# Kernel tuning notes

Measured on AMD Instinct MI355X. Metric: run time of the kernel, lower is better.

## Reference

```python
import jax, jax.numpy as jnp
import numpy as np

DIM = 512
A_HEADS = 8
C_HEADS = 4
DH = 64
EPS = 1e-5


def layer_norm(x, g, b):
    mu = jnp.mean(x, axis=-1, keepdims=True)
    var = jnp.var(x, axis=-1, keepdims=True)
    return (x - mu) * jax.lax.rsqrt(var + EPS) * g + b


def setup_inputs() -> dict:
    key = jax.random.key(0)
    ks = jax.random.split(key, 8)
    inner_a = A_HEADS * DH  # 512
    inner_c = C_HEADS * DH  # 256
    s = 0.02
    return {
        "x": jax.random.normal(ks[0], (4, 192, DIM), dtype=jnp.float32),
        # Attention branch params
        "ln1_g": jnp.ones((DIM,), jnp.float32),
        "ln1_b": jnp.zeros((DIM,), jnp.float32),
        "Wqkv": jax.random.normal(ks[1], (DIM, 3 * inner_a), jnp.float32) * s,
        "Wo": jax.random.normal(ks[2], (inner_a, DIM), jnp.float32) * s,
        "bo": jnp.zeros((DIM,), jnp.float32),
        # Trittention branch params
        "ln2_g": jnp.ones((DIM,), jnp.float32),
        "ln2_b": jnp.zeros((DIM,), jnp.float32),
        "Wabcde": jax.random.normal(ks[3], (DIM, 5 * inner_c), jnp.float32) * s,
        "babcde": jnp.zeros((5 * inner_c,), jnp.float32),
        "Wp": jax.random.normal(ks[4], (inner_c, DIM), jnp.float32) * s,
        "bp": jnp.zeros((DIM,), jnp.float32),
    }


def _attention(x, ln_g, ln_b, Wqkv, Wo, bo):
    B, T, _ = x.shape
    xn = layer_norm(x, ln_g, ln_b)
    qkv = xn @ Wqkv  # [B,T,3*H*D]
    q, k, v = jnp.split(qkv, 3, axis=-1)
    def heads(t):
        return t.reshape(B, T, A_HEADS, DH).transpose(0, 2, 1, 3)  # [B,H,T,D]
    q, k, v = heads(q), heads(k), heads(v)
    scale = DH ** -0.5
    dots = jnp.einsum('bhqd,bhkd->bhqk', q, k) * scale
    attn = jax.nn.softmax(dots, axis=-1)
    out = jnp.einsum('bhqk,bhkd->bhqd', attn, v)
    out = out.transpose(0, 2, 1, 3).reshape(B, T, A_HEADS * DH)
    return out @ Wo + bo


def _trittention(x, ln_g, ln_b, Wabcde, babcde, Wp, bp):
    B, T, _ = x.shape
    xn = layer_norm(x, ln_g, ln_b)
    proj = xn @ Wabcde + babcde  # [B,T,5*H*D]
    a, b_, c, d_, e = jnp.split(proj, 5, axis=-1)
    def heads(t):
        return t.reshape(B, T, C_HEADS, DH)  # [B,T,H,D]
    a, b_, c, d_, e = heads(a), heads(b_), heads(c), heads(d_), heads(e)
    # cubic score: [B,H,S,T,Q]
    score = jnp.einsum('bshd,bthd,bqhd->bhstq', a, b_, c) / DH
    # softmax over joint (s,t) for each query q
    score = score.transpose(0, 1, 4, 2, 3).reshape(B, C_HEADS, T, T * T)
    attn = jax.nn.softmax(score, axis=-1).reshape(B, C_HEADS, T, T, T)
    z = (jnp.einsum('bhqst,bshd->bhqd', attn, d_)
         + jnp.einsum('bhqst,bthd->bhqd', attn, e))
    z = z.transpose(0, 2, 1, 3).reshape(B, T, C_HEADS * DH)
    return z @ Wp + bp


def reference(x, ln1_g, ln1_b, Wqkv, Wo, bo, ln2_g, ln2_b, Wabcde, babcde, Wp, bp):
    return (_attention(x, ln1_g, ln1_b, Wqkv, Wo, bo)
            + _trittention(x, ln2_g, ln2_b, Wabcde, babcde, Wp, bp))
```

## Files before the change

### kernel.cpp

```cpp
#include <hip/hip_runtime.h>
#include <cstdint>


#define B_   4
#define T_   192
#define DIM_ 512
#define AH   8
#define CH   4

typedef unsigned short u16;
typedef unsigned int   u32;
typedef __attribute__((ext_vector_type(8))) short short8;
typedef __attribute__((ext_vector_type(4))) float floatx4;
typedef __attribute__((ext_vector_type(4))) int intx4;
typedef __attribute__((ext_vector_type(2))) float f32x2;
typedef __attribute__((ext_vector_type(8))) _Float16 half8;
typedef __attribute__((ext_vector_type(2))) _Float16 half2v;
typedef __attribute__((ext_vector_type(2))) __fp16 fp16x2;

union Frag  { intx4 i; short8 s; };
union FragH { intx4 i; half8 h; };

__device__ __forceinline__ floatx4 mfma16(Frag a, Frag b, floatx4 c) {
    return __builtin_amdgcn_mfma_f32_16x16x32_bf16(a.s, b.s, c, 0, 0, 0);
}
__device__ __forceinline__ floatx4 mfma16h(FragH a, FragH b, floatx4 c) {
    return __builtin_amdgcn_mfma_f32_16x16x32_f16(a.h, b.h, c, 0, 0, 0);
}

__device__ __forceinline__ float fexp2(float x) {
    return __builtin_amdgcn_exp2f(x);
}

__device__ __forceinline__ float wave_reduce_sum(float v) {
#pragma unroll
    for (int off = 32; off >= 1; off >>= 1)
        v += __shfl_xor(v, off, 64);
    return v;
}

__device__ __forceinline__ u32 pack_rne(float x, float y) {
    u32 ux = __float_as_uint(x);
    u32 uy = __float_as_uint(y);
    ux += 0x7fffu + ((ux >> 16) & 1u);
    uy += 0x7fffu + ((uy >> 16) & 1u);
    return (ux >> 16) | (uy & 0xffff0000u);
}
__device__ __forceinline__ u16 bf16_rne(float x) {
    u32 u = __float_as_uint(x);
    u += 0x7fffu + ((u >> 16) & 1u);
    return (u16)(u >> 16);
}
__device__ __forceinline__ float bf16f(u16 h) { return __uint_as_float(((u32)h) << 16); }

__device__ __forceinline__ u32 pack_f16(float x, float y) {
    union { fp16x2 h; u32 u; } cv;
    cv.h = __builtin_amdgcn_cvt_pkrtz(x, y);
    return cv.u;
}
__device__ __forceinline__ u32 mul_h2(u32 a, u32 b) {
    union { u32 u; half2v h; } ua, ub, uw;
    ua.u = a; ub.u = b;
    uw.h = ua.h * ub.h;
    return uw.u;
}

__device__ __forceinline__ Frag ld_frag8(const u16* p) {
    Frag f;
    uint2 a = *(const uint2*)p;
    uint2 b = *(const uint2*)(p + 4);
    f.i = (intx4){ (int)a.x, (int)a.y, (int)b.x, (int)b.y };
    return f;
}

#define LOG2E 1.44269504088896f

__global__ __launch_bounds__(256) void prep_kernel(
    const float* __restrict__ x,
    const float* __restrict__ g1, const float* __restrict__ b1,
    const float* __restrict__ g2, const float* __restrict__ b2,
    u16* __restrict__ x1h, u16* __restrict__ x1l,
    u16* __restrict__ x2h, u16* __restrict__ x2l,
    const float* __restrict__ Wqkv, u16* __restrict__ wqh,
    const float* __restrict__ Wab,  u16* __restrict__ wah,
    const float* __restrict__ Wo,   const float* __restrict__ Wp,
    u16* __restrict__ wofh, u16* __restrict__ wofl)
{
    __shared__ union { float t[64][65]; float red[4][2]; } u;
    const int tid = threadIdx.x;
    if (blockIdx.x < 768) {
        int row = blockIdx.x;
        const float2 v = ((const float2*)(x + (size_t)row * DIM_))[tid];
        float s  = v.x + v.y;
        float s2 = v.x * v.x + v.y * v.y;
        s  = wave_reduce_sum(s);
        s2 = wave_reduce_sum(s2);
        int w = tid >> 6;
        if ((tid & 63) == 0) { u.red[w][0] = s; u.red[w][1] = s2; }
        __syncthreads();
        float ts  = u.red[0][0] + u.red[1][0] + u.red[2][0] + u.red[3][0];
        float ts2 = u.red[0][1] + u.red[1][1] + u.red[2][1] + u.red[3][1];
        float mean = ts * (1.0f / DIM_);
        float var  = ts2 * (1.0f / DIM_) - mean * mean;
        float rstd = rsqrtf(var + 1e-5f);
        int c0 = tid * 2;
        float n0 = (v.x - mean) * rstd;
        float n1 = (v.y - mean) * rstd;
        float a0 = n0 * g1[c0] + b1[c0], a1 = n1 * g1[c0 + 1] + b1[c0 + 1];
        float c2 = n0 * g2[c0] + b2[c0], c3 = n1 * g2[c0 + 1] + b2[c0 + 1];
        u16 h0 = bf16_rne(a0), h1 = bf16_rne(a1);
        u16 h2 = bf16_rne(c2), h3 = bf16_rne(c3);
        u16 l0 = bf16_rne(a0 - bf16f(h0)), l1 = bf16_rne(a1 - bf16f(h1));
        u16 l2 = bf16_rne(c2 - bf16f(h2)), l3 = bf16_rne(c3 - bf16f(h3));
        size_t o = (size_t)row * 256 + tid;
        ((u32*)x1h)[o] = (u32)h0 | ((u32)h1 << 16);
        ((u32*)x1l)[o] = (u32)l0 | ((u32)l1 << 16);
        ((u32*)x2h)[o] = (u32)h2 | ((u32)h3 << 16);
        ((u32*)x2l)[o] = (u32)l2 | ((u32)l3 << 16);
        return;
    }
    int id = blockIdx.x - 768;
    const float* W; u16 *H, *L; int K, N, Kout, kofs, tile, wantLo;
    if (id < 192)      { W = Wqkv; H = wqh;  L = nullptr; K = 512; N = 1536; Kout = 512; kofs = 0;   tile = id;       wantLo = 0; }
    else if (id < 352) { W = Wab;  H = wah;  L = nullptr; K = 512; N = 1280; Kout = 512; kofs = 0;   tile = id - 192; wantLo = 0; }
    else if (id < 416) { W = Wo;   H = wofh; L = wofl;    K = 512; N = 512;  Kout = 768; kofs = 0;   tile = id - 352; wantLo = 1; }
    else               { W = Wp;   H = wofh; L = wofl;    K = 256; N = 512;  Kout = 768; kofs = 512; tile = id - 416; wantLo = 1; }
    int nx = N >> 6;
    int n0 = (tile % nx) * 64, k0 = (tile / nx) * 64;
    int rr = tid >> 4, c4 = (tid & 15) << 2;
#pragma unroll
    for (int p = 0; p < 4; ++p) {
        int row = rr + p * 16;
        float4 v = *(const float4*)(W + (size_t)(k0 + row) * N + n0 + c4);
        u.t[row][c4 + 0] = v.x; u.t[row][c4 + 1] = v.y;
        u.t[row][c4 + 2] = v.z; u.t[row][c4 + 3] = v.w;
    }
    __syncthreads();
#pragma unroll
    for (int p = 0; p < 4; ++p) {
        int n = rr + p * 16;
        u16 hi[4], lo[4];
#pragma unroll
        for (int c = 0; c < 4; ++c) {
            float v = u.t[c4 + c][n];
            hi[c] = bf16_rne(v);
            lo[c] = bf16_rne(v - bf16f(hi[c]));
        }
        size_t o = (size_t)(n0 + n) * Kout + kofs + k0 + c4;
        *(uint2*)&H[o] = make_uint2((u32)hi[0] | ((u32)hi[1] << 16), (u32)hi[2] | ((u32)hi[3] << 16));
        if (wantLo)
            *(uint2*)&L[o] = make_uint2((u32)lo[0] | ((u32)lo[1] << 16), (u32)lo[2] | ((u32)lo[3] << 16));
    }
}

__global__ __launch_bounds__(256) void gemm_dual(
    const u16* __restrict__ x1h, const u16* __restrict__ x1l,
    const u16* __restrict__ wqh,
    const u16* __restrict__ x2h, const u16* __restrict__ x2l,
    const u16* __restrict__ wah,
    const float* __restrict__ babcde,
    float* __restrict__ qkv, float* __restrict__ proj)
{
    __shared__ u16 As[2][64][68];
    __shared__ u16 Bs[64][68];
    const int tid = threadIdx.x;
    const int nb = blockIdx.x;
    const u16 *Ah, *Al, *BTh; const float* bias; float* C; int N, bn;
    if (nb < 24) { Ah = x1h; Al = x1l; BTh = wqh; bias = nullptr; C = qkv;  N = 1536; bn = nb * 64; }
    else         { Ah = x2h; Al = x2l; BTh = wah; bias = babcde; C = proj; N = 1280; bn = (nb - 24) * 64; }
    const int K = 512;
    const int bm = blockIdx.y * 64;
    const int lane = tid & 63, wave = tid >> 6;
    const int m16 = lane & 15, quad = lane >> 4;
    const int wm = (wave >> 1) * 32, wn = (wave & 1) * 32;
    const int r = tid >> 2, c16 = (tid & 3) * 16;

    floatx4 acc[2][2];
#pragma unroll
    for (int i = 0; i < 2; ++i)
#pragma unroll
        for (int j = 0; j < 2; ++j) acc[i][j] = (floatx4){0.f, 0.f, 0.f, 0.f};

    for (int k0 = 0; k0 < K; k0 += 64) {
        __syncthreads();
        {
            const u16* pa = Ah + (size_t)(bm + r) * K + k0 + c16;
            uint4 v0 = *(const uint4*)pa, v1 = *(const uint4*)(pa + 8);
            *(uint2*)&As[0][r][c16 + 0]  = make_uint2(v0.x, v0.y);
            *(uint2*)&As[0][r][c16 + 4]  = make_uint2(v0.z, v0.w);
            *(uint2*)&As[0][r][c16 + 8]  = make_uint2(v1.x, v1.y);
            *(uint2*)&As[0][r][c16 + 12] = make_uint2(v1.z, v1.w);
            const u16* pl = Al + (size_t)(bm + r) * K + k0 + c16;
            uint4 w0 = *(const uint4*)pl, w1 = *(const uint4*)(pl + 8);
            *(uint2*)&As[1][r][c16 + 0]  = make_uint2(w0.x, w0.y);
            *(uint2*)&As[1][r][c16 + 4]  = make_uint2(w0.z, w0.w);
            *(uint2*)&As[1][r][c16 + 8]  = make_uint2(w1.x, w1.y);
            *(uint2*)&As[1][r][c16 + 12] = make_uint2(w1.z, w1.w);
        }
        {
            const u16* pb = BTh + (size_t)(bn + r) * K + k0 + c16;
            uint4 v0 = *(const uint4*)pb, v1 = *(const uint4*)(pb + 8);
            *(uint2*)&Bs[r][c16 + 0]  = make_uint2(v0.x, v0.y);
            *(uint2*)&Bs[r][c16 + 4]  = make_uint2(v0.z, v0.w);
            *(uint2*)&Bs[r][c16 + 8]  = make_uint2(v1.x, v1.y);
            *(uint2*)&Bs[r][c16 + 12] = make_uint2(v1.z, v1.w);
        }
        __syncthreads();
#pragma unroll
        for (int ks = 0; ks < 2; ++ks) {
            const int ko = ks * 32 + quad * 8;
            Frag a0h = ld_frag8(&As[0][wm + m16][ko]);
            Frag a1h = ld_frag8(&As[0][wm + 16 + m16][ko]);
            Frag a0l = ld_frag8(&As[1][wm + m16][ko]);
            Frag a1l = ld_frag8(&As[1][wm + 16 + m16][ko]);
            Frag b0 = ld_frag8(&Bs[wn + m16][ko]);
            Frag b1 = ld_frag8(&Bs[wn + 16 + m16][ko]);
            acc[0][0] = mfma16(a0h, b0, acc[0][0]);
            acc[0][0] = mfma16(a0l, b0, acc[0][0]);
            acc[0][1] = mfma16(a0h, b1, acc[0][1]);
            acc[0][1] = mfma16(a0l, b1, acc[0][1]);
            acc[1][0] = mfma16(a1h, b0, acc[1][0]);
            acc[1][0] = mfma16(a1l, b0, acc[1][0]);
            acc[1][1] = mfma16(a1h, b1, acc[1][1]);
            acc[1][1] = mfma16(a1l, b1, acc[1][1]);
        }
    }
#pragma unroll
    for (int i = 0; i < 2; ++i)
#pragma unroll
        for (int rr = 0; rr < 4; ++rr) {
            int m = bm + wm + i * 16 + quad * 4 + rr;
#pragma unroll
            for (int j = 0; j < 2; ++j) {
                int n = bn + wn + j * 16 + m16;
                float v = acc[i][j][rr];
                if (bias) v += bias[n];
                C[(size_t)m * N + n] = v;
            }
        }
}

__global__ __launch_bounds__(256) void gemm_epilogue(
    const u16* __restrict__ aoh, const u16* __restrict__ aol,
    const u16* __restrict__ zh,  const u16* __restrict__ zl,
    const u16* __restrict__ BTh, const u16* __restrict__ BTl,
    const float* __restrict__ bo, const float* __restrict__ bp,
    float* __restrict__ C)
{
    __shared__ u16 As[2][32][68];
    __shared__ u16 Bs[2][64][68];
    const int tid = threadIdx.x;
    const int bm = blockIdx.y * 32, bn = blockIdx.x * 64;
    const int lane = tid & 63, wave = tid >> 6;
    const int m16 = lane & 15, quad = lane >> 4;
    const int wm = (wave >> 1) * 16, wn = (wave & 1) * 32;
    const int ra = tid >> 3, c8 = (tid & 7) * 8;
    const int rb = tid >> 2, c16 = (tid & 3) * 16;
    const int N = 512, K = 768;

    floatx4 acc[2];
    acc[0] = (floatx4){0.f, 0.f, 0.f, 0.f};
    acc[1] = (floatx4){0.f, 0.f, 0.f, 0.f};

    for (int k0 = 0; k0 < K; k0 += 64) {
        __syncthreads();
        const u16* pah;
        const u16* pal;
        if (k0 < 512) {
            pah = aoh + (size_t)(bm + ra) * 512 + k0 + c8;
            pal = aol + (size_t)(bm + ra) * 512 + k0 + c8;
        } else {
            pah = zh + (size_t)(bm + ra) * 256 + (k0 - 512) + c8;
            pal = zl + (size_t)(bm + ra) * 256 + (k0 - 512) + c8;
        }
        {
            uint4 v = *(const uint4*)pah;
            *(uint2*)&As[0][ra][c8 + 0] = make_uint2(v.x, v.y);
            *(uint2*)&As[0][ra][c8 + 4] = make_uint2(v.z, v.w);
            uint4 w = *(const uint4*)pal;
            *(uint2*)&As[1][ra][c8 + 0] = make_uint2(w.x, w.y);
            *(uint2*)&As[1][ra][c8 + 4] = make_uint2(w.z, w.w);
        }
        {
            const u16* pb = BTh + (size_t)(bn + rb) * K + k0 + c16;
            uint4 v0 = *(const uint4*)pb, v1 = *(const uint4*)(pb + 8);
            *(uint2*)&Bs[0][rb][c16 + 0]  = make_uint2(v0.x, v0.y);
            *(uint2*)&Bs[0][rb][c16 + 4]  = make_uint2(v0.z, v0.w);
            *(uint2*)&Bs[0][rb][c16 + 8]  = make_uint2(v1.x, v1.y);
            *(uint2*)&Bs[0][rb][c16 + 12] = make_uint2(v1.z, v1.w);
            const u16* pc = BTl + (size_t)(bn + rb) * K + k0 + c16;
            uint4 w0 = *(const uint4*)pc, w1 = *(const uint4*)(pc + 8);
            *(uint2*)&Bs[1][rb][c16 + 0]  = make_uint2(w0.x, w0.y);
            *(uint2*)&Bs[1][rb][c16 + 4]  = make_uint2(w0.z, w0.w);
            *(uint2*)&Bs[1][rb][c16 + 8]  = make_uint2(w1.x, w1.y);
            *(uint2*)&Bs[1][rb][c16 + 12] = make_uint2(w1.z, w1.w);
        }
        __syncthreads();
#pragma unroll
        for (int ks = 0; ks < 2; ++ks) {
            const int ko = ks * 32 + quad * 8;
            Frag ah = ld_frag8(&As[0][wm + m16][ko]);
            Frag al = ld_frag8(&As[1][wm + m16][ko]);
            Frag b0h = ld_frag8(&Bs[0][wn + m16][ko]);
            Frag b1h = ld_frag8(&Bs[0][wn + 16 + m16][ko]);
            Frag b0l = ld_frag8(&Bs[1][wn + m16][ko]);
            Frag b1l = ld_frag8(&Bs[1][wn + 16 + m16][ko]);
            acc[0] = mfma16(ah, b0h, acc[0]);
            acc[0] = mfma16(al, b0h, acc[0]);
            acc[0] = mfma16(ah, b0l, acc[0]);
            acc[1] = mfma16(ah, b1h, acc[1]);
            acc[1] = mfma16(al, b1h, acc[1]);
            acc[1] = mfma16(ah, b1l, acc[1]);
        }
    }
#pragma unroll
    for (int rr = 0; rr < 4; ++rr) {
        int m = bm + wm + quad * 4 + rr;
#pragma unroll
        for (int j = 0; j < 2; ++j) {
            int n = bn + wn + j * 16 + m16;
            C[(size_t)m * N + n] = acc[j][rr] + bo[n] + bp[n];
        }
    }
}

__global__ __launch_bounds__(256) void attn_mfma(
    const float* __restrict__ qkv, u16* __restrict__ aoh, u16* __restrict__ aol)
{
    __shared__ union { u16 Ks[192][68]; u16 P[64][196]; } KP;
    __shared__ u16 Vt[64][196];
    const int qt = blockIdx.x, h = blockIdx.y, b = blockIdx.z;
    const int tid = threadIdx.x;
    const int lane = tid & 63, wave = tid >> 6;
    const int m16 = lane & 15, quad = lane >> 4;
    const size_t base = (size_t)(b * T_) * 1536 + h * 64;

    for (int i = tid; i < 192 * 16; i += 256) {
        int row = i >> 4, c4 = (i & 15) << 2;
        float4 kv = *(const float4*)(qkv + base + (size_t)row * 1536 + 512 + c4);
        *(uint2*)&KP.Ks[row][c4] = make_uint2(pack_rne(kv.x, kv.y), pack_rne(kv.z, kv.w));
        float4 vv = *(const float4*)(qkv + base + (size_t)row * 1536 + 1024 + c4);
        Vt[c4 + 0][row] = bf16_rne(vv.x);
        Vt[c4 + 1][row] = bf16_rne(vv.y);
        Vt[c4 + 2][row] = bf16_rne(vv.z);
        Vt[c4 + 3][row] = bf16_rne(vv.w);
    }

    Frag qf0, qf1;
    {
        const float s = 0.125f * LOG2E;
        const float* qp = qkv + base + (size_t)(qt * 64 + wave * 16 + m16) * 1536 + quad * 8;
        float4 u0 = *(const float4*)qp;
        float4 u1 = *(const float4*)(qp + 4);
        float4 u2 = *(const float4*)(qp + 32);
        float4 u3 = *(const float4*)(qp + 36);
        qf0.i = (intx4){ (int)pack_rne(u0.x * s, u0.y * s), (int)pack_rne(u0.z * s, u0.w * s),
                         (int)pack_rne(u1.x * s, u1.y * s), (int)pack_rne(u1.z * s, u1.w * s) };
        qf1.i = (intx4){ (int)pack_rne(u2.x * s, u2.y * s), (int)pack_rne(u2.z * s, u2.w * s),
                         (int)pack_rne(u3.x * s, u3.y * s), (int)pack_rne(u3.z * s, u3.w * s) };
    }
    __syncthreads();

    float ev[12][4];
    float rsum[4] = {0.f, 0.f, 0.f, 0.f};
#pragma unroll
    for (int tt = 0; tt < 12; ++tt) {
        Frag kb0 = ld_frag8(&KP.Ks[tt * 16 + m16][quad * 8]);
        Frag kb1 = ld_frag8(&KP.Ks[tt * 16 + m16][32 + quad * 8]);
        floatx4 accs = (floatx4){0.f, 0.f, 0.f, 0.f};
        accs = mfma16(qf0, kb0, accs);
        accs = mfma16(qf1, kb1, accs);
#pragma unroll
        for (int rr = 0; rr < 4; ++rr) {
            float e = fexp2(accs[rr]);
            ev[tt][rr] = e;
            rsum[rr] += e;
        }
    }
#pragma unroll
    for (int rr = 0; rr < 4; ++rr) {
        float v = rsum[rr];
        v += __shfl_xor(v, 1, 64);
        v += __shfl_xor(v, 2, 64);
        v += __shfl_xor(v, 4, 64);
        v += __shfl_xor(v, 8, 64);
        rsum[rr] = 1.0f / v;
    }

    __syncthreads();
#pragma unroll
    for (int tt = 0; tt < 12; ++tt)
#pragma unroll
        for (int rr = 0; rr < 4; ++rr)
            KP.P[wave * 16 + quad * 4 + rr][tt * 16 + m16] = bf16_rne(ev[tt][rr]);

    floatx4 acco[4];
#pragma unroll
    for (int dt = 0; dt < 4; ++dt) acco[dt] = (floatx4){0.f, 0.f, 0.f, 0.f};
#pragma unroll
    for (int ts = 0; ts < 6; ++ts) {
        Frag pf = ld_frag8(&KP.P[wave * 16 + m16][ts * 32 + quad * 8]);
#pragma unroll
        for (int dt = 0; dt < 4; ++dt) {
            Frag vf = ld_frag8(&Vt[dt * 16 + m16][ts * 32 + quad * 8]);
            acco[dt] = mfma16(pf, vf, acco[dt]);
        }
    }
#pragma unroll
    for (int dt = 0; dt < 4; ++dt)
#pragma unroll
        for (int rr = 0; rr < 4; ++rr) {
            float o = acco[dt][rr] * rsum[rr];
            size_t idx = (size_t)(b * T_ + qt * 64 + wave * 16 + quad * 4 + rr) * 512
                       + h * 64 + dt * 16 + m16;
            u16 hi = bf16_rne(o);
            aoh[idx] = hi;
            aol[idx] = bf16_rne(o - bf16f(hi));
        }
}

__global__ __launch_bounds__(256, 3) void tritt_score_mfma(
    const float* __restrict__ proj, float* __restrict__ rs_g, float* __restrict__ rt_g)
{
    __shared__ u32 a_lds[48 * 36];
    __shared__ u32 b_lds[48 * 36];
    __shared__ float rs_lds[48][33];
    __shared__ float rt_lds[48][33];

    const int h = blockIdx.y, b = blockIdx.z;
    const int qt = blockIdx.x >> 4;
    const int sc = (blockIdx.x >> 2) & 3;
    const int tc = blockIdx.x & 3;
    const int q0 = qt * 32, s0 = sc * 48, t0 = tc * 48;
    const int tid  = threadIdx.x;
    const int lane = tid & 63, wave = tid >> 6;
    const int m16  = lane & 15, quad = lane >> 4;
    const int bh = b * CH + h;
    const size_t rowbase = (size_t)(b * T_) * 1280 + h * 64;
    const float kA = 0.015625f * LOG2E;

    for (int i = tid; i < 48 * 32; i += 256) {
        int row = i >> 5, cp = i & 31;
        const float2 va = *(const float2*)(proj + rowbase + (size_t)(s0 + row) * 1280 + 0 + cp * 2);
        a_lds[row * 36 + cp] = pack_f16(va.x * kA, va.y * kA);
        const float2 vb = *(const float2*)(proj + rowbase + (size_t)(t0 + row) * 1280 + 256 + cp * 2);
        b_lds[row * 36 + cp] = pack_f16(vb.x, vb.y);
    }

    FragH cf[2][2];
#pragma unroll
    for (int jq = 0; jq < 2; ++jq) {
        const float* cp = proj + rowbase + (size_t)(q0 + jq * 16 + m16) * 1280 + 512 + quad * 8;
        float4 u0 = *(const float4*)(cp);
        float4 u1 = *(const float4*)(cp + 4);
        float4 u2 = *(const float4*)(cp + 32);
        float4 u3 = *(const float4*)(cp + 36);
        cf[jq][0].i = (intx4){ (int)pack_f16(u0.x, u0.y), (int)pack_f16(u0.z, u0.w),
                               (int)pack_f16(u1.x, u1.y), (int)pack_f16(u1.z, u1.w) };
        cf[jq][1].i = (intx4){ (int)pack_f16(u2.x, u2.y), (int)pack_f16(u2.z, u2.w),
                               (int)pack_f16(u3.x, u3.y), (int)pack_f16(u3.z, u3.w) };
    }
    __syncthreads();

    float rt_acc[3][4][2] = {};

    for (int si = 0; si < 12; ++si) {
        const int srow = wave * 12 + si;
        const intx4 av0 = *(const intx4*)(a_lds + srow * 36 + quad * 4);
        const intx4 av1 = *(const intx4*)(a_lds + srow * 36 + 16 + quad * 4);
        float rs_s[2] = {0.f, 0.f};
#pragma unroll
        for (int tt = 0; tt < 3; ++tt) {
            const u32* bp = b_lds + (tt * 16 + m16) * 36;
            intx4 bv0 = *(const intx4*)(bp + quad * 4);
            intx4 bv1 = *(const intx4*)(bp + 16 + quad * 4);
            FragH w0, w1;
#pragma unroll
            for (int j = 0; j < 4; ++j) {
                w0.i[j] = (int)mul_h2((u32)av0[j], (u32)bv0[j]);
                w1.i[j] = (int)mul_h2((u32)av1[j], (u32)bv1[j]);
            }
#pragma unroll
            for (int jq = 0; jq < 2; ++jq) {
                floatx4 acc = (floatx4){0.f, 0.f, 0.f, 0.f};
                acc = mfma16h(w0, cf[jq][0], acc);
                acc = mfma16h(w1, cf[jq][1], acc);
#pragma unroll
                for (int rr = 0; rr < 4; ++rr) {
                    float e = fexp2(acc[rr]);
                    rt_acc[tt][rr][jq] += e;
                    rs_s[jq] += e;
                }
            }
        }
#pragma unroll
        for (int jq = 0; jq < 2; ++jq) {
            float v = rs_s[jq];
            v += __shfl_xor(v, 16, 64);
            v += __shfl_xor(v, 32, 64);
            if (lane < 16) rs_lds[srow][jq * 16 + m16] = v;
        }
    }

    __syncthreads();
    for (int w = 0; w < 4; ++w) {
        if (wave == w) {
#pragma unroll
            for (int tt = 0; tt < 3; ++tt)
#pragma unroll
                for (int rr = 0; rr < 4; ++rr) {
                    int t = tt * 16 + quad * 4 + rr;
#pragma unroll
                    for (int jq = 0; jq < 2; ++jq) {
                        if (w == 0) rt_lds[t][jq * 16 + m16] = rt_acc[tt][rr][jq];
                        else        rt_lds[t][jq * 16 + m16] += rt_acc[tt][rr][jq];
                    }
                }
        }
        __syncthreads();
    }
    for (int i = tid; i < 32 * 48; i += 256) {
        int qq = i / 48, ss = i - qq * 48;
        rs_g[((size_t)(tc * 16 + bh) * T_ + q0 + qq) * T_ + s0 + ss] = rs_lds[ss][qq];
    }
    for (int i = tid; i < 32 * 48; i += 256) {
        int qq = i / 48, t2 = i - qq * 48;
        rt_g[((size_t)(sc * 16 + bh) * T_ + q0 + qq) * T_ + t0 + t2] = rt_lds[t2][qq];
    }
}

__global__ __launch_bounds__(256) void zgemm(
    const float* __restrict__ rs_g, const float* __restrict__ rt_g,
    const float* __restrict__ proj, u16* __restrict__ zzh, u16* __restrict__ zzl)
{
    __shared__ u16 As[2][64][68];
    __shared__ u16 Bs[32][68];
    __shared__ float zred[64][4];
    __shared__ float Zl[64];
    const int mt = blockIdx.x >> 1, dh2 = blockIdx.x & 1, bh = blockIdx.y;
    const int b = bh >> 2, h = bh & 3;
    const int q0 = mt * 64;
    const int tid = threadIdx.x;
    const int lane = tid & 63, wave = tid >> 6;
    const int m16 = lane & 15, quad = lane >> 4;
    const int wm = (wave >> 1) * 32, wn = (wave & 1) * 16;
    const int r = tid >> 2, c16 = (tid & 3) * 16;

    {
        float zp = 0.f;
        const int j = tid & 3;
#pragma unroll
        for (int tc = 0; tc < 4; ++tc) {
            const float* p = rs_g + ((size_t)(tc * 16 + bh) * T_ + q0 + r) * T_ + j * 48;
#pragma unroll
            for (int s = 0; s < 48; s += 4) {
                float4 v = *(const float4*)(p + s);
                zp += (v.x + v.y) + (v.z + v.w);
            }
        }
        zred[r][j] = zp;
    }
    __syncthreads();
    if (tid < 64)
        Zl[tid] = 1.0f / (zred[tid][0] + zred[tid][1] + zred[tid][2] + zred[tid][3]);

    floatx4 acc[2];
    acc[0] = (floatx4){0.f, 0.f, 0.f, 0.f};
    acc[1] = (floatx4){0.f, 0.f, 0.f, 0.f};

    for (int k0 = 0; k0 < 384; k0 += 64) {
        __syncthreads();
        {
            float g[16];
#pragma unroll
            for (int i = 0; i < 16; ++i) g[i] = 0.f;
            if (k0 < 192) {
#pragma unroll
                for (int tc = 0; tc < 4; ++tc) {
                    const float* p = rs_g + ((size_t)(tc * 16 + bh) * T_ + q0 + r) * T_ + k0 + c16;
#pragma unroll
                    for (int i = 0; i < 16; i += 4) {
                        float4 v = *(const float4*)(p + i);
                        g[i] += v.x; g[i + 1] += v.y; g[i + 2] += v.z; g[i + 3] += v.w;
                    }
                }
            } else {
#pragma unroll
                for (int sc = 0; sc < 4; ++sc) {
                    const float* p = rt_g + ((size_t)(sc * 16 + bh) * T_ + q0 + r) * T_ + (k0 - 192) + c16;
#pragma unroll
                    for (int i = 0; i < 16; i += 4) {
                        float4 v = *(const float4*)(p + i);
                        g[i] += v.x; g[i + 1] += v.y; g[i + 2] += v.z; g[i + 3] += v.w;
                    }
                }
            }
#pragma unroll
            for (int i = 0; i < 16; ++i) {
                u16 hi = bf16_rne(g[i]);
                As[0][r][c16 + i] = hi;
                As[1][r][c16 + i] = bf16_rne(g[i] - bf16f(hi));
            }
        }
        {
            const int colbase = (k0 < 192 ? 768 : 1024) + h * 64 + dh2 * 32;
            const int s0 = (k0 < 192 ? k0 : k0 - 192);
            const int sl = tid >> 2;
            const int d4b = (tid & 3) * 4;
#pragma unroll
            for (int i = 0; i < 2; ++i) {
                int dd = d4b + i * 16;
                float4 v = *(const float4*)(proj + (size_t)(b * T_ + s0 + sl) * 1280 + colbase + dd);
                Bs[dd + 0][sl] = bf16_rne(v.x);
                Bs[dd + 1][sl] = bf16_rne(v.y);
                Bs[dd + 2][sl] = bf16_rne(v.z);
                Bs[dd + 3][sl] = bf16_rne(v.w);
            }
        }
        __syncthreads();
#pragma unroll
        for (int ks = 0; ks < 2; ++ks) {
            const int ko = ks * 32 + quad * 8;
            Frag g0h = ld_frag8(&As[0][wm + m16][ko]);
            Frag g1h = ld_frag8(&As[0][wm + 16 + m16][ko]);
            Frag g0l = ld_frag8(&As[1][wm + m16][ko]);
            Frag g1l = ld_frag8(&As[1][wm + 16 + m16][ko]);
            Frag d0 = ld_frag8(&Bs[wn + m16][ko]);
            acc[0] = mfma16(g0h, d0, acc[0]);
            acc[0] = mfma16(g0l, d0, acc[0]);
            acc[1] = mfma16(g1h, d0, acc[1]);
            acc[1] = mfma16(g1l, d0, acc[1]);
        }
    }
#pragma unroll
    for (int i = 0; i < 2; ++i)
#pragma unroll
        for (int rr = 0; rr < 4; ++rr) {
            int m = wm + i * 16 + quad * 4 + rr;
            int d = dh2 * 32 + wn + m16;
            float zv = acc[i][rr] * Zl[m];
            size_t idx = (size_t)(b * T_ + q0 + m) * 256 + h * 64 + d;
            u16 hi = bf16_rne(zv);
            zzh[idx] = hi;
            zzl[idx] = bf16_rne(zv - bf16f(hi));
        }
}

extern "C" void kernel_launch(void* const* d_in, const int* in_sizes, int n_in,
                              void* d_out, int out_size, void* d_ws, size_t ws_size,
                              hipStream_t stream)
{
    const float* x      = (const float*)d_in[0];
    const float* ln1_g  = (const float*)d_in[1];
    const float* ln1_b  = (const float*)d_in[2];
    const float* Wqkv   = (const float*)d_in[3];
    const float* Wo     = (const float*)d_in[4];
    const float* bo     = (const float*)d_in[5];
    const float* ln2_g  = (const float*)d_in[6];
    const float* ln2_b  = (const float*)d_in[7];
    const float* Wabcde = (const float*)d_in[8];
    const float* babcde = (const float*)d_in[9];
    const float* Wp     = (const float*)d_in[10];
    const float* bp     = (const float*)d_in[11];
    float* out = (float*)d_out;

    float* ws   = (float*)d_ws;
    float* proj = ws;
    u16* wofh   = (u16*)(proj + 983040);
    u16* wofl   = wofh + 393216;
    u16* aoh    = (u16*)(ws + 1376256);
    u16* aol    = aoh + 393216;
    u16* zh     = (u16*)(ws + 1769472);
    u16* zl     = zh + 196608;
    float* rs   = ws + 1966080;
    float* rt   = rs + 2359296;
    float* qkv = rs;
    u16* x1h = (u16*)(rs + 1179648);
    u16* x1l = x1h + 393216;
    u16* x2h = x1l + 393216;
    u16* x2l = x2h + 393216;
    u16* wqh = (u16*)rt;
    u16* wah = wqh + 786432;

    prep_kernel<<<1216, 256, 0, stream>>>(x, ln1_g, ln1_b, ln2_g, ln2_b,
                                          x1h, x1l, x2h, x2l,
                                          Wqkv, wqh, Wabcde, wah,
                                          Wo, Wp, wofh, wofl);
    gemm_dual<<<dim3(44, 12), 256, 0, stream>>>(x1h, x1l, wqh, x2h, x2l, wah,
                                                babcde, qkv, proj);
    attn_mfma<<<dim3(3, AH, B_), 256, 0, stream>>>(qkv, aoh, aol);
    tritt_score_mfma<<<dim3(96, CH, B_), 256, 0, stream>>>(proj, rs, rt);
    zgemm<<<dim3(6, 16), 256, 0, stream>>>(rs, rt, proj, zh, zl);
    gemm_epilogue<<<dim3(8, 24), 256, 0, stream>>>(aoh, aol, zh, zl, wofh, wofl, bo, bp, out);
}
```

Baseline: 167.7 us.

## Split attention keys across wave pairs and halve query tile per block

Each attention block now handles 32 queries instead of 64. The four waves split into two query groups times two key halves, with each wave computing partial PV products over 96 keys. The partial outputs and row sums are merged through shared memory, which is reused via a union with Vt. This doubles the grid from 96 to 192 blocks so more CUs are busy. The cost is that K and V loads are duplicated per block, and an extra merge step adds syncs.

```diff
diff --git a/kernel.cpp b/kernel.cpp
--- a/kernel.cpp
+++ b/kernel.cpp
@@ -327,12 +327,14 @@
 __global__ __launch_bounds__(256) void attn_mfma(
     const float* __restrict__ qkv, u16* __restrict__ aoh, u16* __restrict__ aol)
 {
-    __shared__ union { u16 Ks[192][68]; u16 P[64][196]; } KP;
-    __shared__ u16 Vt[64][196];
+    __shared__ union { u16 Ks[192][68]; u16 P[32][196]; } KP;
+    __shared__ union { u16 Vt[64][196]; struct { float m[2][16][68]; float r[2][16]; } mg; } VU;
     const int qt = blockIdx.x, h = blockIdx.y, b = blockIdx.z;
     const int tid = threadIdx.x;
     const int lane = tid & 63, wave = tid >> 6;
     const int m16 = lane & 15, quad = lane >> 4;
+    const int qg = wave & 1;
+    const int kh = wave >> 1;
     const size_t base = (size_t)(b * T_) * 1536 + h * 64;
 
     for (int i = tid; i < 192 * 16; i += 256) {
@@ -340,16 +342,16 @@
         float4 kv = *(const float4*)(qkv + base + (size_t)row * 1536 + 512 + c4);
         *(uint2*)&KP.Ks[row][c4] = make_uint2(pack_rne(kv.x, kv.y), pack_rne(kv.z, kv.w));
         float4 vv = *(const float4*)(qkv + base + (size_t)row * 1536 + 1024 + c4);
-        Vt[c4 + 0][row] = bf16_rne(vv.x);
-        Vt[c4 + 1][row] = bf16_rne(vv.y);
-        Vt[c4 + 2][row] = bf16_rne(vv.z);
-        Vt[c4 + 3][row] = bf16_rne(vv.w);
+        VU.Vt[c4 + 0][row] = bf16_rne(vv.x);
+        VU.Vt[c4 + 1][row] = bf16_rne(vv.y);
+        VU.Vt[c4 + 2][row] = bf16_rne(vv.z);
+        VU.Vt[c4 + 3][row] = bf16_rne(vv.w);
     }
 
     Frag qf0, qf1;
     {
         const float s = 0.125f * LOG2E;
-        const float* qp = qkv + base + (size_t)(qt * 64 + wave * 16 + m16) * 1536 + quad * 8;
+        const float* qp = qkv + base + (size_t)(qt * 32 + qg * 16 + m16) * 1536 + quad * 8;
         float4 u0 = *(const float4*)qp;
         float4 u1 = *(const float4*)(qp + 4);
         float4 u2 = *(const float4*)(qp + 32);
@@ -361,12 +363,13 @@
     }
     __syncthreads();
 
-    float ev[12][4];
+    float ev[6][4];
     float rsum[4] = {0.f, 0.f, 0.f, 0.f};
 #pragma unroll
-    for (int tt = 0; tt < 12; ++tt) {
-        Frag kb0 = ld_frag8(&KP.Ks[tt * 16 + m16][quad * 8]);
-        Frag kb1 = ld_frag8(&KP.Ks[tt * 16 + m16][32 + quad * 8]);
+    for (int tt = 0; tt < 6; ++tt) {
+        const int krow = kh * 96 + tt * 16 + m16;
+        Frag kb0 = ld_frag8(&KP.Ks[krow][quad * 8]);
+        Frag kb1 = ld_frag8(&KP.Ks[krow][32 + quad * 8]);
         floatx4 accs = (floatx4){0.f, 0.f, 0.f, 0.f};
         accs = mfma16(qf0, kb0, accs);
         accs = mfma16(qf1, kb1, accs);
@@ -384,39 +387,60 @@
         v += __shfl_xor(v, 2, 64);
         v += __shfl_xor(v, 4, 64);
         v += __shfl_xor(v, 8, 64);
-        rsum[rr] = 1.0f / v;
+        rsum[rr] = v;
     }
 
     __syncthreads();
 #pragma unroll
-    for (int tt = 0; tt < 12; ++tt)
+    for (int tt = 0; tt < 6; ++tt)
 #pragma unroll
         for (int rr = 0; rr < 4; ++rr)
-            KP.P[wave * 16 + quad * 4 + rr][tt * 16 + m16] = bf16_rne(ev[tt][rr]);
+            KP.P[qg * 16 + quad * 4 + rr][kh * 96 + tt * 16 + m16] = bf16_rne(ev[tt][rr]);
 
     floatx4 acco[4];
 #pragma unroll
     for (int dt = 0; dt < 4; ++dt) acco[dt] = (floatx4){0.f, 0.f, 0.f, 0.f};
 #pragma unroll
-    for (int ts = 0; ts < 6; ++ts) {
-        Frag pf = ld_frag8(&KP.P[wave * 16 + m16][ts * 32 + quad * 8]);
+    for (int ts = 0; ts < 3; ++ts) {
+        Frag pf = ld_frag8(&KP.P[qg * 16 + m16][kh * 96 + ts * 32 + quad * 8]);
 #pragma unroll
         for (int dt = 0; dt < 4; ++dt) {
-            Frag vf = ld_frag8(&Vt[dt * 16 + m16][ts * 32 + quad * 8]);
+            Frag vf = ld_frag8(&VU.Vt[dt * 16 + m16][kh * 96 + ts * 32 + quad * 8]);
             acco[dt] = mfma16(pf, vf, acco[dt]);
         }
     }
-#pragma unroll
-    for (int dt = 0; dt < 4; ++dt)
-#pragma unroll
-        for (int rr = 0; rr < 4; ++rr) {
-            float o = acco[dt][rr] * rsum[rr];
-            size_t idx = (size_t)(b * T_ + qt * 64 + wave * 16 + quad * 4 + rr) * 512
-                       + h * 64 + dt * 16 + m16;
-            u16 hi = bf16_rne(o);
-            aoh[idx] = hi;
-            aol[idx] = bf16_rne(o - bf16f(hi));
-        }
+
+    __syncthreads();
+    if (kh == 1) {
+#pragma unroll
+        for (int dt = 0; dt < 4; ++dt)
+#pragma unroll
+            for (int rr = 0; rr < 4; ++rr)
+                VU.mg.m[qg][quad * 4 + rr][dt * 16 + m16] = acco[dt][rr];
+        if (m16 == 0) {
+#pragma unroll
+            for (int rr = 0; rr < 4; ++rr)
+                VU.mg.r[qg][quad * 4 + rr] = rsum[rr];
+        }
+    }
+    __syncthreads();
+    if (kh == 0) {
+        float rinv[4];
+#pragma unroll
+        for (int rr = 0; rr < 4; ++rr)
+            rinv[rr] = 1.0f / (rsum[rr] + VU.mg.r[qg][quad * 4 + rr]);
+#pragma unroll
+        for (int dt = 0; dt < 4; ++dt)
+#pragma unroll
+            for (int rr = 0; rr < 4; ++rr) {
+                float o = (acco[dt][rr] + VU.mg.m[qg][quad * 4 + rr][dt * 16 + m16]) * rinv[rr];
+                size_t idx = (size_t)(b * T_ + qt * 32 + qg * 16 + quad * 4 + rr) * 512
+                           + h * 64 + dt * 16 + m16;
+                u16 hi = bf16_rne(o);
+                aoh[idx] = hi;
+                aol[idx] = bf16_rne(o - bf16f(hi));
+            }
+    }
 }
 
 __global__ __launch_bounds__(256, 3) void tritt_score_mfma(
@@ -688,7 +712,7 @@
                                           Wo, Wp, wofh, wofl);
     gemm_dual<<<dim3(44, 12), 256, 0, stream>>>(x1h, x1l, wqh, x2h, x2l, wah,
                                                 babcde, qkv, proj);
-    attn_mfma<<<dim3(3, AH, B_), 256, 0, stream>>>(qkv, aoh, aol);
+    attn_mfma<<<dim3(6, AH, B_), 256, 0, stream>>>(qkv, aoh, aol);
     tritt_score_mfma<<<dim3(96, CH, B_), 256, 0, stream>>>(proj, rs, rt);
     zgemm<<<dim3(6, 16), 256, 0, stream>>>(rs, rt, proj, zh, zl);
     gemm_epilogue<<<dim3(8, 24), 256, 0, stream>>>(aoh, aol, zh, zl, wofh, wofl, bo, bp, out);
```

Result: no change. 167.9 us (+0.1%).
